# Performance work log

Measured on AMD Instinct MI355X. Metric: run time of the kernel, lower is better.

Reference implementation:

```python
import jax, jax.numpy as jnp
import numpy as np

D_MODEL = 1024
N_EXPERTS = 8
TOP_K = 2
LN_EPS = 1e-5


def setup_inputs() -> dict:
    key = jax.random.key(0)
    ks = jax.random.split(key, 8)
    B, S, d, E = 2, 2048, D_MODEL, N_EXPERTS
    f = 2 * d
    s_in = 0.02
    return {
        "x": jax.random.normal(ks[0], (B, S, d), jnp.float32),
        "Wg": jax.random.normal(ks[1], (d, E), jnp.float32) * s_in,
        "bg": jnp.zeros((E,), jnp.float32),
        "W1": jax.random.normal(ks[2], (E, d, f), jnp.float32) * s_in,
        "b1": jnp.zeros((E, f), jnp.float32),
        "W2": jax.random.normal(ks[3], (E, f, d), jnp.float32) * s_in,
        "b2": jnp.zeros((E, d), jnp.float32),
        "gamma": jnp.ones((d,), jnp.float32),
        "beta": jnp.zeros((d,), jnp.float32),
    }


def reference(x, Wg, bg, W1, b1, W2, b2, gamma, beta):
    # Gating + top-k routing (softmax over the selected top-k logits only)
    logits = jnp.einsum("bsd,de->bse", x, Wg) + bg            # [B,S,E]
    topk_vals, topk_idx = jax.lax.top_k(logits, TOP_K)         # [B,S,K]
    topk_w = jax.nn.softmax(topk_vals, axis=-1)                # [B,S,K]

    # Expert MLPs evaluated densely for all experts (dropout is identity in eval)
    h = jax.nn.relu(jnp.einsum("bsd,edf->bsef", x, W1) + b1)   # [B,S,E,2d]
    eo = jnp.einsum("bsef,efd->bsed", h, W2) + b2              # [B,S,E,d]

    # Gather the top-k experts' outputs per token and combine with gate weights
    sel = jnp.take_along_axis(eo, topk_idx[..., None], axis=2)  # [B,S,K,d]
    mixed = jnp.sum(sel * topk_w[..., None], axis=2)            # [B,S,d]

    # Residual + LayerNorm
    y = mixed + x
    mu = jnp.mean(y, axis=-1, keepdims=True)
    var = jnp.mean(jnp.square(y - mu), axis=-1, keepdims=True)
    return gamma * (y - mu) * jax.lax.rsqrt(var + LN_EPS) + beta
```

## Files before the change

kernel.cpp:

```cpp
#include <hip/hip_runtime.h>


typedef unsigned short ushort_t;
typedef short short8 __attribute__((ext_vector_type(8)));
typedef float f32x4 __attribute__((ext_vector_type(4)));

#define T_TOKENS 4096
#define DMODEL 1024
#define FFN 2048
#define NEXP 8
#define MAXSLOTS 9216
#define GATE_BLOCKS 256
#define TOK_PER_BLK 16
#define MAX_MT 12

__device__ __forceinline__ ushort_t f2bf(float f) {
    unsigned u = __float_as_uint(f);
    return (ushort_t)((u + 0x7fffu + ((u >> 16) & 1u)) >> 16);
}
__device__ __forceinline__ float bflo(unsigned packed) {
    return __uint_as_float(packed << 16);
}
__device__ __forceinline__ float bfhi(unsigned packed) {
    return __uint_as_float(packed & 0xffff0000u);
}

__device__ __forceinline__ void gload_lds16(const void* g, void* l) {
    __builtin_amdgcn_global_load_lds(
        (const __attribute__((address_space(1))) unsigned int*)g,
        (__attribute__((address_space(3))) unsigned int*)l,
        16, 0, 0);
}

__global__ __launch_bounds__(256) void gate_kernel(
    const float* __restrict__ x, const float* __restrict__ Wg,
    const float* __restrict__ bg,
    int* __restrict__ top_idx, float* __restrict__ top_w,
    int* __restrict__ blk_hist)
{
    __shared__ int hist[NEXP];
    const int tid = threadIdx.x, lane = tid & 63, w = tid >> 6;
    if (tid < NEXP) hist[tid] = 0;
    __syncthreads();

    float wreg[16][8];
    #pragma unroll
    for (int i = 0; i < 16; i++) {
        const float4* wp = (const float4*)&Wg[(i * 64 + lane) * 8];
        float4 a = wp[0], b = wp[1];
        wreg[i][0] = a.x; wreg[i][1] = a.y; wreg[i][2] = a.z; wreg[i][3] = a.w;
        wreg[i][4] = b.x; wreg[i][5] = b.y; wreg[i][6] = b.z; wreg[i][7] = b.w;
    }
    float bgv[8];
    #pragma unroll
    for (int e = 0; e < 8; e++) bgv[e] = bg[e];

    const int t0 = blockIdx.x * TOK_PER_BLK + w * 4;
    #pragma unroll 1
    for (int it = 0; it < 4; it++) {
        int t = t0 + it;
        const float* xr = x + (size_t)t * DMODEL;
        float acc[8] = {0.f,0.f,0.f,0.f,0.f,0.f,0.f,0.f};
        #pragma unroll
        for (int i = 0; i < 16; i++) {
            float xv = xr[i * 64 + lane];
            #pragma unroll
            for (int e = 0; e < 8; e++) acc[e] += xv * wreg[i][e];
        }
        #pragma unroll
        for (int off = 32; off > 0; off >>= 1) {
            #pragma unroll
            for (int e = 0; e < 8; e++) acc[e] += __shfl_down(acc[e], off);
        }
        if (lane == 0) {
            float l[8];
            #pragma unroll
            for (int e = 0; e < 8; e++) l[e] = acc[e] + bgv[e];
            int i0 = 0; float v0 = l[0];
            #pragma unroll
            for (int e = 1; e < 8; e++) if (l[e] > v0) { v0 = l[e]; i0 = e; }
            int i1 = -1; float v1 = -1e30f;
            #pragma unroll
            for (int e = 0; e < 8; e++) if (e != i0 && l[e] > v1) { v1 = l[e]; i1 = e; }
            float eg = expf(v1 - v0);
            float den = 1.f + eg;
            int p0 = atomicAdd(&hist[i0], 1);
            int p1 = atomicAdd(&hist[i1], 1);
            top_idx[2 * t]     = i0 | (p0 << 4);
            top_idx[2 * t + 1] = i1 | (p1 << 4);
            top_w[2 * t]     = 1.f / den;
            top_w[2 * t + 1] = eg / den;
        }
    }
    __syncthreads();
    if (tid < NEXP) blk_hist[blockIdx.x * NEXP + tid] = hist[tid];
}

__global__ __launch_bounds__(512) void scan_kernel(
    const int* __restrict__ blk_hist, int* __restrict__ blk_base,
    int* __restrict__ offs)
{
    __shared__ int cnt[NEXP];
    const int tid = threadIdx.x, lane = tid & 63, e = tid >> 6;
    int carry = 0;
    #pragma unroll
    for (int r = 0; r < GATE_BLOCKS / 64; r++) {
        int b = r * 64 + lane;
        int orig = blk_hist[b * NEXP + e];
        int v = orig;
        #pragma unroll
        for (int off = 1; off < 64; off <<= 1) {
            int u = __shfl_up(v, off);
            if (lane >= off) v += u;
        }
        blk_base[b * NEXP + e] = carry + v - orig;
        carry += __shfl(v, 63);
    }
    if (lane == 0) cnt[e] = carry;
    __syncthreads();
    if (tid == 0) {
        int cum = 0;
        for (int ee = 0; ee < NEXP; ee++) {
            offs[ee] = cum;
            cum += (cnt[ee] + 127) & ~127;
        }
        offs[NEXP] = cum;
    }
}

__global__ __launch_bounds__(256) void scatter_gather_kernel(
    const float* __restrict__ x, const int* __restrict__ top_idx,
    const int* __restrict__ offs, const int* __restrict__ blk_base,
    int* __restrict__ slot_of, ushort_t* __restrict__ Xg)
{
    const int t = blockIdx.x, tid = threadIdx.x;
    __shared__ int slots[2];
    if (tid < 2) {
        int v = top_idx[2 * t + tid];
        int e = v & 15, pos = v >> 4;
        int gb = t / TOK_PER_BLK;
        int slot = offs[e] + blk_base[gb * NEXP + e] + pos;
        slot_of[2 * t + tid] = slot;
        slots[tid] = slot;
    }
    __syncthreads();
    float4 xv = ((const float4*)(x + (size_t)t * DMODEL))[tid];
    uint2 pk;
    pk.x = f2bf(xv.x) | ((unsigned)f2bf(xv.y) << 16);
    pk.y = f2bf(xv.z) | ((unsigned)f2bf(xv.w) << 16);
    ((uint2*)(Xg + (size_t)slots[0] * DMODEL))[tid] = pk;
    ((uint2*)(Xg + (size_t)slots[1] * DMODEL))[tid] = pk;
}

__global__ __launch_bounds__(256) void transpose_kernel(
    const float* __restrict__ W1, const float* __restrict__ W2,
    ushort_t* __restrict__ W1T, ushort_t* __restrict__ W2T)
{
    int b = blockIdx.x;
    const float* s; ushort_t* d; int Rs, Cs, rt, ct;
    if (b < 4096) {
        int e = b >> 9, t = b & 511;
        rt = t >> 5; ct = t & 31;
        s = W1 + (size_t)e * DMODEL * FFN;
        d = W1T + (size_t)e * DMODEL * FFN;
        Rs = DMODEL; Cs = FFN;
    } else {
        b -= 4096;
        int e = b >> 9, t = b & 511;
        rt = t >> 4; ct = t & 15;
        s = W2 + (size_t)e * DMODEL * FFN;
        d = W2T + (size_t)e * DMODEL * FFN;
        Rs = FFN; Cs = DMODEL;
    }
    const int r0 = rt * 64, c0 = ct * 64;
    const int ty = threadIdx.x & 15, tx = threadIdx.x >> 4;

    float v[4][4];
    #pragma unroll
    for (int i = 0; i < 4; i++) {
        float4 ld = *(const float4*)&s[(size_t)(r0 + ty * 4 + i) * Cs + c0 + tx * 4];
        v[i][0] = ld.x; v[i][1] = ld.y; v[i][2] = ld.z; v[i][3] = ld.w;
    }
    #pragma unroll
    for (int j = 0; j < 4; j++) {
        uint2 pk;
        pk.x = f2bf(v[0][j]) | ((unsigned)f2bf(v[1][j]) << 16);
        pk.y = f2bf(v[2][j]) | ((unsigned)f2bf(v[3][j]) << 16);
        *(uint2*)&d[(size_t)(c0 + tx * 4 + j) * Rs + r0 + ty * 4] = pk;
    }
}

template <int K, int N, bool RELU>
__global__ __launch_bounds__(256) void expert_gemm(
    const ushort_t* __restrict__ A,
    const ushort_t* __restrict__ Bt,
    const float* __restrict__ bias,
    ushort_t* __restrict__ Cout,
    const int* __restrict__ offs)
{
    const int e  = blockIdx.x;
    const int nt = blockIdx.y;
    const int mt = blockIdx.z;
    const int off_e = offs[e];
    const int Mpad  = offs[e + 1] - off_e;
    if (mt * 128 >= Mpad) return;

    __shared__ __align__(16) ushort_t As[128 * 32];
    __shared__ __align__(16) ushort_t Bs[128 * 32];

    const int tid  = threadIdx.x;
    const int lane = tid & 63;
    const int w    = tid >> 6;
    const int quad = lane >> 4;
    const int r16  = lane & 15;
    const int lrow = lane >> 2;
    const int lk   = (((lane & 3) ^ ((lane >> 3) & 3))) * 8;

    const size_t arow0 = (size_t)(off_e + mt * 128);
    const ushort_t* aS0 = A + (arow0 + (size_t)(2 * w + 0) * 16 + lrow) * K + lk;
    const ushort_t* aS1 = A + (arow0 + (size_t)(2 * w + 1) * 16 + lrow) * K + lk;
    const ushort_t* Bte = Bt + (size_t)e * N * K;
    const ushort_t* bS0 = Bte + ((size_t)(nt * 128 + (2 * w + 0) * 16 + lrow)) * K + lk;
    const ushort_t* bS1 = Bte + ((size_t)(nt * 128 + (2 * w + 1) * 16 + lrow)) * K + lk;
    ushort_t* aD0 = &As[(2 * w + 0) * 512];
    ushort_t* aD1 = &As[(2 * w + 1) * 512];
    ushort_t* bD0 = &Bs[(2 * w + 0) * 512];
    ushort_t* bD1 = &Bs[(2 * w + 1) * 512];

    const int wm = (w >> 1) * 64;
    const int wn = (w & 1) * 64;
    const int sw = ((r16 >> 1) & 3) ^ quad;

    f32x4 acc[4][4];
    #pragma unroll
    for (int i = 0; i < 4; i++)
        #pragma unroll
        for (int j = 0; j < 4; j++)
            acc[i][j] = (f32x4){0.f, 0.f, 0.f, 0.f};

    for (int k0 = 0; k0 < K; k0 += 32) {
        gload_lds16(aS0 + k0, aD0);
        gload_lds16(aS1 + k0, aD1);
        gload_lds16(bS0 + k0, bD0);
        gload_lds16(bS1 + k0, bD1);
        __syncthreads();
        short8 af[4], bfr[4];
        #pragma unroll
        for (int i = 0; i < 4; i++)
            af[i] = *(const short8*)&As[(wm + i * 16 + r16) * 32 + sw * 8];
        #pragma unroll
        for (int j = 0; j < 4; j++)
            bfr[j] = *(const short8*)&Bs[(wn + j * 16 + r16) * 32 + sw * 8];
        #pragma unroll
        for (int i = 0; i < 4; i++)
            #pragma unroll
            for (int j = 0; j < 4; j++)
                acc[i][j] = __builtin_amdgcn_mfma_f32_16x16x32_bf16(
                    af[i], bfr[j], acc[i][j], 0, 0, 0);
        __syncthreads();
    }

    const float* be = bias + (size_t)e * N;
    #pragma unroll
    for (int i = 0; i < 4; i++) {
        #pragma unroll
        for (int j = 0; j < 4; j++) {
            int n = nt * 128 + wn + j * 16 + r16;
            float bv = be[n];
            #pragma unroll
            for (int r = 0; r < 4; r++) {
                int m = mt * 128 + wm + i * 16 + quad * 4 + r;
                float v = acc[i][j][r] + bv;
                if (RELU) v = v > 0.f ? v : 0.f;
                Cout[(size_t)(off_e + m) * N + n] = f2bf(v);
            }
        }
    }
}

__global__ __launch_bounds__(256) void ln_kernel(
    const float* __restrict__ x, const ushort_t* __restrict__ O,
    const int* __restrict__ slot_of, const float* __restrict__ top_w,
    const float* __restrict__ gamma, const float* __restrict__ beta,
    float* __restrict__ out)
{
    int t = blockIdx.x, tid = threadIdx.x;
    int s0 = slot_of[2 * t], s1 = slot_of[2 * t + 1];
    float w0 = top_w[2 * t], w1 = top_w[2 * t + 1];
    float4 xv = ((const float4*)(x + (size_t)t * DMODEL))[tid];
    uint2 a = ((const uint2*)(O + (size_t)s0 * DMODEL))[tid];
    uint2 b = ((const uint2*)(O + (size_t)s1 * DMODEL))[tid];

    float y[4];
    y[0] = xv.x + w0 * bflo(a.x) + w1 * bflo(b.x);
    y[1] = xv.y + w0 * bfhi(a.x) + w1 * bfhi(b.x);
    y[2] = xv.z + w0 * bflo(a.y) + w1 * bflo(b.y);
    y[3] = xv.w + w0 * bfhi(a.y) + w1 * bfhi(b.y);

    float s = y[0] + y[1] + y[2] + y[3];
    float sq = y[0]*y[0] + y[1]*y[1] + y[2]*y[2] + y[3]*y[3];
    __shared__ float red[2][4];
    #pragma unroll
    for (int off = 32; off > 0; off >>= 1) {
        s += __shfl_down(s, off);
        sq += __shfl_down(sq, off);
    }
    int lane = tid & 63, wv = tid >> 6;
    if (lane == 0) { red[0][wv] = s; red[1][wv] = sq; }
    __syncthreads();
    if (tid == 0) {
        float S = red[0][0] + red[0][1] + red[0][2] + red[0][3];
        float SQ = red[1][0] + red[1][1] + red[1][2] + red[1][3];
        float mu = S * (1.f / DMODEL);
        float var = SQ * (1.f / DMODEL) - mu * mu;
        red[0][0] = mu;
        red[1][0] = rsqrtf(var + 1e-5f);
    }
    __syncthreads();
    float mu = red[0][0], inv = red[1][0];
    float4 gv = ((const float4*)gamma)[tid];
    float4 bv = ((const float4*)beta)[tid];
    float4 ov;
    ov.x = gv.x * (y[0] - mu) * inv + bv.x;
    ov.y = gv.y * (y[1] - mu) * inv + bv.y;
    ov.z = gv.z * (y[2] - mu) * inv + bv.z;
    ov.w = gv.w * (y[3] - mu) * inv + bv.w;
    ((float4*)(out + (size_t)t * DMODEL))[tid] = ov;
}

extern "C" void kernel_launch(void* const* d_in, const int* in_sizes, int n_in,
                              void* d_out, int out_size, void* d_ws, size_t ws_size,
                              hipStream_t stream)
{
    const float* x     = (const float*)d_in[0];
    const float* Wg    = (const float*)d_in[1];
    const float* bg    = (const float*)d_in[2];
    const float* W1    = (const float*)d_in[3];
    const float* b1    = (const float*)d_in[4];
    const float* W2    = (const float*)d_in[5];
    const float* b2    = (const float*)d_in[6];
    const float* gamma = (const float*)d_in[7];
    const float* beta  = (const float*)d_in[8];
    float* out = (float*)d_out;

    char* ws = (char*)d_ws;
    size_t o = 0;
    auto alloc = [&](size_t bytes) {
        size_t r = o;
        o = (o + bytes + 255) & ~(size_t)255;
        return r;
    };
    size_t o_offs    = alloc((NEXP + 1) * 4);
    size_t o_topidx  = alloc((size_t)T_TOKENS * 2 * 4);
    size_t o_topw    = alloc((size_t)T_TOKENS * 2 * 4);
    size_t o_slotof  = alloc((size_t)T_TOKENS * 2 * 4);
    size_t o_bhist   = alloc((size_t)GATE_BLOCKS * NEXP * 4);
    size_t o_bbase   = alloc((size_t)GATE_BLOCKS * NEXP * 4);
    size_t o_w1t     = alloc((size_t)NEXP * DMODEL * FFN * 2);
    size_t o_w2t     = alloc((size_t)NEXP * DMODEL * FFN * 2);
    size_t o_xg      = alloc((size_t)MAXSLOTS * DMODEL * 2);
    size_t o_h       = alloc((size_t)MAXSLOTS * FFN * 2);
    size_t o_obuf    = alloc((size_t)MAXSLOTS * DMODEL * 2);
    (void)ws_size; (void)in_sizes; (void)n_in; (void)out_size;

    int*      offs     = (int*)(ws + o_offs);
    int*      top_idx  = (int*)(ws + o_topidx);
    float*    top_w    = (float*)(ws + o_topw);
    int*      slot_of  = (int*)(ws + o_slotof);
    int*      blk_hist = (int*)(ws + o_bhist);
    int*      blk_base = (int*)(ws + o_bbase);
    ushort_t* W1T      = (ushort_t*)(ws + o_w1t);
    ushort_t* W2T      = (ushort_t*)(ws + o_w2t);
    ushort_t* Xg       = (ushort_t*)(ws + o_xg);
    ushort_t* H        = (ushort_t*)(ws + o_h);
    ushort_t* Obuf     = (ushort_t*)(ws + o_obuf);

    gate_kernel<<<GATE_BLOCKS, 256, 0, stream>>>(x, Wg, bg, top_idx, top_w, blk_hist);
    transpose_kernel<<<8192, 256, 0, stream>>>(W1, W2, W1T, W2T);
    scan_kernel<<<1, 512, 0, stream>>>(blk_hist, blk_base, offs);
    scatter_gather_kernel<<<T_TOKENS, 256, 0, stream>>>(x, top_idx, offs, blk_base, slot_of, Xg);
    expert_gemm<DMODEL, FFN, true>
        <<<dim3(NEXP, FFN / 128, MAX_MT), 256, 0, stream>>>(Xg, W1T, b1, H, offs);
    expert_gemm<FFN, DMODEL, false>
        <<<dim3(NEXP, DMODEL / 128, MAX_MT), 256, 0, stream>>>(H, W2T, b2, Obuf, offs);
    ln_kernel<<<T_TOKENS, 256, 0, stream>>>(x, Obuf, slot_of, top_w, gamma, beta, out);
}
```

Measured before the change: 315.4 us.

## Fuse weight transpose, routing scan and token scatter into one kernel

Merges the weight transpose, the single-block scan and the token scatter/gather into one launch. Each scatter block now redoes the full 256-block histogram reduction itself to get expert offsets and its own prefix, so the serial one-block scan kernel and the blk_base buffer go away. This removes two launches and the serial scan bubble, and lets the scatter work overlap with the transpose blocks. In exchange every token block repeats a small redundant reduction over the histogram.

```diff
diff --git a/kernel.cpp b/kernel.cpp
--- a/kernel.cpp
+++ b/kernel.cpp
@@ -96,98 +96,113 @@
     if (tid < NEXP) blk_hist[blockIdx.x * NEXP + tid] = hist[tid];
 }
 
-__global__ __launch_bounds__(512) void scan_kernel(
-    const int* __restrict__ blk_hist, int* __restrict__ blk_base,
-    int* __restrict__ offs)
-{
-    __shared__ int cnt[NEXP];
-    const int tid = threadIdx.x, lane = tid & 63, e = tid >> 6;
-    int carry = 0;
-    #pragma unroll
-    for (int r = 0; r < GATE_BLOCKS / 64; r++) {
-        int b = r * 64 + lane;
-        int orig = blk_hist[b * NEXP + e];
-        int v = orig;
-        #pragma unroll
-        for (int off = 1; off < 64; off <<= 1) {
-            int u = __shfl_up(v, off);
-            if (lane >= off) v += u;
-        }
-        blk_base[b * NEXP + e] = carry + v - orig;
-        carry += __shfl(v, 63);
-    }
-    if (lane == 0) cnt[e] = carry;
+__global__ __launch_bounds__(256) void mid_kernel(
+    const float* __restrict__ W1, const float* __restrict__ W2,
+    ushort_t* __restrict__ W1T, ushort_t* __restrict__ W2T,
+    const float* __restrict__ x, const int* __restrict__ top_idx,
+    const int* __restrict__ blk_hist,
+    int* __restrict__ offs_out, int* __restrict__ slot_of,
+    ushort_t* __restrict__ Xg)
+{
+    int b = blockIdx.x;
+    if (b < 8192) {
+        const float* s; ushort_t* d; int Rs, Cs, rt, ct;
+        if (b < 4096) {
+            int e = b >> 9, t = b & 511;
+            rt = t >> 5; ct = t & 31;
+            s = W1 + (size_t)e * DMODEL * FFN;
+            d = W1T + (size_t)e * DMODEL * FFN;
+            Rs = DMODEL; Cs = FFN;
+        } else {
+            int bb = b - 4096;
+            int e = bb >> 9, t = bb & 511;
+            rt = t >> 4; ct = t & 15;
+            s = W2 + (size_t)e * DMODEL * FFN;
+            d = W2T + (size_t)e * DMODEL * FFN;
+            Rs = FFN; Cs = DMODEL;
+        }
+        const int r0 = rt * 64, c0 = ct * 64;
+        const int ty = threadIdx.x & 15, tx = threadIdx.x >> 4;
+
+        float v[4][4];
+        #pragma unroll
+        for (int i = 0; i < 4; i++) {
+            float4 ld = *(const float4*)&s[(size_t)(r0 + ty * 4 + i) * Cs + c0 + tx * 4];
+            v[i][0] = ld.x; v[i][1] = ld.y; v[i][2] = ld.z; v[i][3] = ld.w;
+        }
+        #pragma unroll
+        for (int j = 0; j < 4; j++) {
+            uint2 pk;
+            pk.x = f2bf(v[0][j]) | ((unsigned)f2bf(v[1][j]) << 16);
+            pk.y = f2bf(v[2][j]) | ((unsigned)f2bf(v[3][j]) << 16);
+            *(uint2*)&d[(size_t)(c0 + tx * 4 + j) * Rs + r0 + ty * 4] = pk;
+        }
+        return;
+    }
+
+    const int t = b - 8192;
+    const int tid = threadIdx.x, lane = tid & 63, w = tid >> 6;
+    const int gb = t / TOK_PER_BLK;
+
+    __shared__ int red_tot[4][NEXP];
+    __shared__ int red_pre[4][NEXP];
+    __shared__ int tot8[NEXP], pre8[NEXP];
+    __shared__ int slots_sh[2];
+
+    int4 h0 = ((const int4*)&blk_hist[tid * NEXP])[0];
+    int4 h1 = ((const int4*)&blk_hist[tid * NEXP])[1];
+    int tot[8] = {h0.x, h0.y, h0.z, h0.w, h1.x, h1.y, h1.z, h1.w};
+    int pre[8];
+    int lt = (tid < gb) ? 1 : 0;
+    #pragma unroll
+    for (int e = 0; e < 8; e++) pre[e] = lt ? tot[e] : 0;
+    #pragma unroll
+    for (int off = 32; off > 0; off >>= 1) {
+        #pragma unroll
+        for (int e = 0; e < 8; e++) {
+            tot[e] += __shfl_down(tot[e], off);
+            pre[e] += __shfl_down(pre[e], off);
+        }
+    }
+    if (lane == 0) {
+        #pragma unroll
+        for (int e = 0; e < 8; e++) { red_tot[w][e] = tot[e]; red_pre[w][e] = pre[e]; }
+    }
+    __syncthreads();
+    if (tid < NEXP) {
+        tot8[tid] = red_tot[0][tid] + red_tot[1][tid] + red_tot[2][tid] + red_tot[3][tid];
+        pre8[tid] = red_pre[0][tid] + red_pre[1][tid] + red_pre[2][tid] + red_pre[3][tid];
+    }
     __syncthreads();
     if (tid == 0) {
+        int offsl[NEXP + 1];
         int cum = 0;
-        for (int ee = 0; ee < NEXP; ee++) {
-            offs[ee] = cum;
-            cum += (cnt[ee] + 127) & ~127;
-        }
-        offs[NEXP] = cum;
-    }
-}
-
-__global__ __launch_bounds__(256) void scatter_gather_kernel(
-    const float* __restrict__ x, const int* __restrict__ top_idx,
-    const int* __restrict__ offs, const int* __restrict__ blk_base,
-    int* __restrict__ slot_of, ushort_t* __restrict__ Xg)
-{
-    const int t = blockIdx.x, tid = threadIdx.x;
-    __shared__ int slots[2];
-    if (tid < 2) {
-        int v = top_idx[2 * t + tid];
-        int e = v & 15, pos = v >> 4;
-        int gb = t / TOK_PER_BLK;
-        int slot = offs[e] + blk_base[gb * NEXP + e] + pos;
-        slot_of[2 * t + tid] = slot;
-        slots[tid] = slot;
+        #pragma unroll
+        for (int e = 0; e < 8; e++) {
+            offsl[e] = cum;
+            cum += (tot8[e] + 127) & ~127;
+        }
+        offsl[NEXP] = cum;
+        #pragma unroll
+        for (int k = 0; k < 2; k++) {
+            int v = top_idx[2 * t + k];
+            int e = v & 15, pos = v >> 4;
+            int slot = offsl[e] + pre8[e] + pos;
+            slot_of[2 * t + k] = slot;
+            slots_sh[k] = slot;
+        }
+        if (t == 0) {
+            #pragma unroll
+            for (int e = 0; e <= NEXP; e++) offs_out[e] = offsl[e];
+        }
     }
     __syncthreads();
     float4 xv = ((const float4*)(x + (size_t)t * DMODEL))[tid];
     uint2 pk;
     pk.x = f2bf(xv.x) | ((unsigned)f2bf(xv.y) << 16);
     pk.y = f2bf(xv.z) | ((unsigned)f2bf(xv.w) << 16);
-    ((uint2*)(Xg + (size_t)slots[0] * DMODEL))[tid] = pk;
-    ((uint2*)(Xg + (size_t)slots[1] * DMODEL))[tid] = pk;
-}
-
-__global__ __launch_bounds__(256) void transpose_kernel(
-    const float* __restrict__ W1, const float* __restrict__ W2,
-    ushort_t* __restrict__ W1T, ushort_t* __restrict__ W2T)
-{
-    int b = blockIdx.x;
-    const float* s; ushort_t* d; int Rs, Cs, rt, ct;
-    if (b < 4096) {
-        int e = b >> 9, t = b & 511;
-        rt = t >> 5; ct = t & 31;
-        s = W1 + (size_t)e * DMODEL * FFN;
-        d = W1T + (size_t)e * DMODEL * FFN;
-        Rs = DMODEL; Cs = FFN;
-    } else {
-        b -= 4096;
-        int e = b >> 9, t = b & 511;
-        rt = t >> 4; ct = t & 15;
-        s = W2 + (size_t)e * DMODEL * FFN;
-        d = W2T + (size_t)e * DMODEL * FFN;
-        Rs = FFN; Cs = DMODEL;
-    }
-    const int r0 = rt * 64, c0 = ct * 64;
-    const int ty = threadIdx.x & 15, tx = threadIdx.x >> 4;
-
-    float v[4][4];
-    #pragma unroll
-    for (int i = 0; i < 4; i++) {
-        float4 ld = *(const float4*)&s[(size_t)(r0 + ty * 4 + i) * Cs + c0 + tx * 4];
-        v[i][0] = ld.x; v[i][1] = ld.y; v[i][2] = ld.z; v[i][3] = ld.w;
-    }
-    #pragma unroll
-    for (int j = 0; j < 4; j++) {
-        uint2 pk;
-        pk.x = f2bf(v[0][j]) | ((unsigned)f2bf(v[1][j]) << 16);
-        pk.y = f2bf(v[2][j]) | ((unsigned)f2bf(v[3][j]) << 16);
-        *(uint2*)&d[(size_t)(c0 + tx * 4 + j) * Rs + r0 + ty * 4] = pk;
-    }
+    ((uint2*)(Xg + (size_t)slots_sh[0] * DMODEL))[tid] = pk;
+    ((uint2*)(Xg + (size_t)slots_sh[1] * DMODEL))[tid] = pk;
 }
 
 template <int K, int N, bool RELU>
@@ -355,7 +370,6 @@
     size_t o_topw    = alloc((size_t)T_TOKENS * 2 * 4);
     size_t o_slotof  = alloc((size_t)T_TOKENS * 2 * 4);
     size_t o_bhist   = alloc((size_t)GATE_BLOCKS * NEXP * 4);
-    size_t o_bbase   = alloc((size_t)GATE_BLOCKS * NEXP * 4);
     size_t o_w1t     = alloc((size_t)NEXP * DMODEL * FFN * 2);
     size_t o_w2t     = alloc((size_t)NEXP * DMODEL * FFN * 2);
     size_t o_xg      = alloc((size_t)MAXSLOTS * DMODEL * 2);
@@ -368,7 +382,6 @@
     float*    top_w    = (float*)(ws + o_topw);
     int*      slot_of  = (int*)(ws + o_slotof);
     int*      blk_hist = (int*)(ws + o_bhist);
-    int*      blk_base = (int*)(ws + o_bbase);
     ushort_t* W1T      = (ushort_t*)(ws + o_w1t);
     ushort_t* W2T      = (ushort_t*)(ws + o_w2t);
     ushort_t* Xg       = (ushort_t*)(ws + o_xg);
@@ -376,9 +389,8 @@
     ushort_t* Obuf     = (ushort_t*)(ws + o_obuf);
 
     gate_kernel<<<GATE_BLOCKS, 256, 0, stream>>>(x, Wg, bg, top_idx, top_w, blk_hist);
-    transpose_kernel<<<8192, 256, 0, stream>>>(W1, W2, W1T, W2T);
-    scan_kernel<<<1, 512, 0, stream>>>(blk_hist, blk_base, offs);
-    scatter_gather_kernel<<<T_TOKENS, 256, 0, stream>>>(x, top_idx, offs, blk_base, slot_of, Xg);
+    mid_kernel<<<8192 + T_TOKENS, 256, 0, stream>>>(
+        W1, W2, W1T, W2T, x, top_idx, blk_hist, offs, slot_of, Xg);
     expert_gemm<DMODEL, FFN, true>
         <<<dim3(NEXP, FFN / 128, MAX_MT), 256, 0, stream>>>(Xg, W1T, b1, H, offs);
     expert_gemm<FFN, DMODEL, false>
```

Result: slower. 325.0 us (+3.1%).

## Pre-tile expert weights into contiguous 128x32 blocks and spread gating over more blocks

Applied to the files above, without the earlier changes.

The weight conversion kernel now writes each expert weight into contiguous 128x32 bf16 tiles, ordered exactly as the GEMM consumes them. Each K-step's B load is therefore one contiguous 8KB chunk instead of 128 strided rows. This also makes the conversion's writes local, where before they were widely strided transposed stores. Separately, the gate kernel now gives each warp one token over 1024 blocks, instead of looping over four tokens in 256 blocks, to raise parallelism; the trade-off is more per-block histogram entries for the scan to process.

```diff
diff --git a/kernel.cpp b/kernel.cpp
--- a/kernel.cpp
+++ b/kernel.cpp
@@ -10,8 +10,8 @@
 #define FFN 2048
 #define NEXP 8
 #define MAXSLOTS 9216
-#define GATE_BLOCKS 256
-#define TOK_PER_BLK 16
+#define GATE_BLOCKS 1024
+#define TOK_PER_BLK 4
 #define MAX_MT 12
 
 __device__ __forceinline__ ushort_t f2bf(float f) {
@@ -55,42 +55,38 @@
     #pragma unroll
     for (int e = 0; e < 8; e++) bgv[e] = bg[e];
 
-    const int t0 = blockIdx.x * TOK_PER_BLK + w * 4;
-    #pragma unroll 1
-    for (int it = 0; it < 4; it++) {
-        int t = t0 + it;
-        const float* xr = x + (size_t)t * DMODEL;
-        float acc[8] = {0.f,0.f,0.f,0.f,0.f,0.f,0.f,0.f};
-        #pragma unroll
-        for (int i = 0; i < 16; i++) {
-            float xv = xr[i * 64 + lane];
-            #pragma unroll
-            for (int e = 0; e < 8; e++) acc[e] += xv * wreg[i][e];
-        }
-        #pragma unroll
-        for (int off = 32; off > 0; off >>= 1) {
-            #pragma unroll
-            for (int e = 0; e < 8; e++) acc[e] += __shfl_down(acc[e], off);
-        }
-        if (lane == 0) {
-            float l[8];
-            #pragma unroll
-            for (int e = 0; e < 8; e++) l[e] = acc[e] + bgv[e];
-            int i0 = 0; float v0 = l[0];
-            #pragma unroll
-            for (int e = 1; e < 8; e++) if (l[e] > v0) { v0 = l[e]; i0 = e; }
-            int i1 = -1; float v1 = -1e30f;
-            #pragma unroll
-            for (int e = 0; e < 8; e++) if (e != i0 && l[e] > v1) { v1 = l[e]; i1 = e; }
-            float eg = expf(v1 - v0);
-            float den = 1.f + eg;
-            int p0 = atomicAdd(&hist[i0], 1);
-            int p1 = atomicAdd(&hist[i1], 1);
-            top_idx[2 * t]     = i0 | (p0 << 4);
-            top_idx[2 * t + 1] = i1 | (p1 << 4);
-            top_w[2 * t]     = 1.f / den;
-            top_w[2 * t + 1] = eg / den;
-        }
+    const int t = blockIdx.x * TOK_PER_BLK + w;
+    const float* xr = x + (size_t)t * DMODEL;
+    float acc[8] = {0.f,0.f,0.f,0.f,0.f,0.f,0.f,0.f};
+    #pragma unroll
+    for (int i = 0; i < 16; i++) {
+        float xv = xr[i * 64 + lane];
+        #pragma unroll
+        for (int e = 0; e < 8; e++) acc[e] += xv * wreg[i][e];
+    }
+    #pragma unroll
+    for (int off = 32; off > 0; off >>= 1) {
+        #pragma unroll
+        for (int e = 0; e < 8; e++) acc[e] += __shfl_down(acc[e], off);
+    }
+    if (lane == 0) {
+        float l[8];
+        #pragma unroll
+        for (int e = 0; e < 8; e++) l[e] = acc[e] + bgv[e];
+        int i0 = 0; float v0 = l[0];
+        #pragma unroll
+        for (int e = 1; e < 8; e++) if (l[e] > v0) { v0 = l[e]; i0 = e; }
+        int i1 = -1; float v1 = -1e30f;
+        #pragma unroll
+        for (int e = 0; e < 8; e++) if (e != i0 && l[e] > v1) { v1 = l[e]; i1 = e; }
+        float eg = expf(v1 - v0);
+        float den = 1.f + eg;
+        int p0 = atomicAdd(&hist[i0], 1);
+        int p1 = atomicAdd(&hist[i1], 1);
+        top_idx[2 * t]     = i0 | (p0 << 4);
+        top_idx[2 * t + 1] = i1 | (p1 << 4);
+        top_w[2 * t]     = 1.f / den;
+        top_w[2 * t + 1] = eg / den;
     }
     __syncthreads();
     if (tid < NEXP) blk_hist[blockIdx.x * NEXP + tid] = hist[tid];
@@ -152,33 +148,34 @@
     ((uint2*)(Xg + (size_t)slots[1] * DMODEL))[tid] = pk;
 }
 
-__global__ __launch_bounds__(256) void transpose_kernel(
+__global__ __launch_bounds__(256) void tiler_kernel(
     const float* __restrict__ W1, const float* __restrict__ W2,
     ushort_t* __restrict__ W1T, ushort_t* __restrict__ W2T)
 {
     int b = blockIdx.x;
-    const float* s; ushort_t* d; int Rs, Cs, rt, ct;
+    const float* s; ushort_t* dtile; int Cs, nt, kt, ktiles;
     if (b < 4096) {
         int e = b >> 9, t = b & 511;
-        rt = t >> 5; ct = t & 31;
+        nt = t >> 5; kt = t & 31; ktiles = 32;
         s = W1 + (size_t)e * DMODEL * FFN;
-        d = W1T + (size_t)e * DMODEL * FFN;
-        Rs = DMODEL; Cs = FFN;
+        dtile = W1T + (size_t)e * DMODEL * FFN + (size_t)(nt * ktiles + kt) * 4096;
+        Cs = FFN;
     } else {
-        b -= 4096;
-        int e = b >> 9, t = b & 511;
-        rt = t >> 4; ct = t & 15;
+        int bb = b - 4096;
+        int e = bb >> 9, t = bb & 511;
+        nt = t >> 6; kt = t & 63; ktiles = 64;
         s = W2 + (size_t)e * DMODEL * FFN;
-        d = W2T + (size_t)e * DMODEL * FFN;
-        Rs = FFN; Cs = DMODEL;
-    }
-    const int r0 = rt * 64, c0 = ct * 64;
-    const int ty = threadIdx.x & 15, tx = threadIdx.x >> 4;
+        dtile = W2T + (size_t)e * DMODEL * FFN + (size_t)(nt * ktiles + kt) * 4096;
+        Cs = DMODEL;
+    }
+    const int lc = threadIdx.x & 31;
+    const int g  = threadIdx.x >> 5;
 
     float v[4][4];
     #pragma unroll
     for (int i = 0; i < 4; i++) {
-        float4 ld = *(const float4*)&s[(size_t)(r0 + ty * 4 + i) * Cs + c0 + tx * 4];
+        float4 ld = *(const float4*)&s[(size_t)(kt * 32 + g * 4 + i) * Cs
+                                       + nt * 128 + lc * 4];
         v[i][0] = ld.x; v[i][1] = ld.y; v[i][2] = ld.z; v[i][3] = ld.w;
     }
     #pragma unroll
@@ -186,7 +183,7 @@
         uint2 pk;
         pk.x = f2bf(v[0][j]) | ((unsigned)f2bf(v[1][j]) << 16);
         pk.y = f2bf(v[2][j]) | ((unsigned)f2bf(v[3][j]) << 16);
-        *(uint2*)&d[(size_t)(c0 + tx * 4 + j) * Rs + r0 + ty * 4] = pk;
+        *(uint2*)&dtile[(4 * lc + j) * 32 + g * 4] = pk;
     }
 }
 
@@ -219,9 +216,9 @@
     const size_t arow0 = (size_t)(off_e + mt * 128);
     const ushort_t* aS0 = A + (arow0 + (size_t)(2 * w + 0) * 16 + lrow) * K + lk;
     const ushort_t* aS1 = A + (arow0 + (size_t)(2 * w + 1) * 16 + lrow) * K + lk;
-    const ushort_t* Bte = Bt + (size_t)e * N * K;
-    const ushort_t* bS0 = Bte + ((size_t)(nt * 128 + (2 * w + 0) * 16 + lrow)) * K + lk;
-    const ushort_t* bS1 = Bte + ((size_t)(nt * 128 + (2 * w + 1) * 16 + lrow)) * K + lk;
+    const ushort_t* Bte = Bt + (size_t)e * N * K + (size_t)nt * 128 * K;
+    const ushort_t* bS0 = Bte + ((2 * w + 0) * 16 + lrow) * 32 + lk;
+    const ushort_t* bS1 = Bte + ((2 * w + 1) * 16 + lrow) * 32 + lk;
     ushort_t* aD0 = &As[(2 * w + 0) * 512];
     ushort_t* aD1 = &As[(2 * w + 1) * 512];
     ushort_t* bD0 = &Bs[(2 * w + 0) * 512];
@@ -241,8 +238,8 @@
     for (int k0 = 0; k0 < K; k0 += 32) {
         gload_lds16(aS0 + k0, aD0);
         gload_lds16(aS1 + k0, aD1);
-        gload_lds16(bS0 + k0, bD0);
-        gload_lds16(bS1 + k0, bD1);
+        gload_lds16(bS0 + (size_t)k0 * 128, bD0);
+        gload_lds16(bS1 + (size_t)k0 * 128, bD1);
         __syncthreads();
         short8 af[4], bfr[4];
         #pragma unroll
@@ -376,7 +373,7 @@
     ushort_t* Obuf     = (ushort_t*)(ws + o_obuf);
 
     gate_kernel<<<GATE_BLOCKS, 256, 0, stream>>>(x, Wg, bg, top_idx, top_w, blk_hist);
-    transpose_kernel<<<8192, 256, 0, stream>>>(W1, W2, W1T, W2T);
+    tiler_kernel<<<8192, 256, 0, stream>>>(W1, W2, W1T, W2T);
     scan_kernel<<<1, 512, 0, stream>>>(blk_hist, blk_base, offs);
     scatter_gather_kernel<<<T_TOKENS, 256, 0, stream>>>(x, top_idx, offs, blk_base, slot_of, Xg);
     expert_gemm<DMODEL, FFN, true>
```

New measurement: 316.4 us. Within noise of the previous version (+0.3%).
